# Optimization experiments

Hardware: AMD Instinct MI355X
Metric: run time of the kernel (lower is better)

Reference implementation:

```python
import jax, jax.numpy as jnp
import numpy as np

SHIFT_MIN, SHIFT_MAX = -14.0, 0.0  # weight_bits=5 -> (-(2^4-2), 0)
FRAC_BITS = 16
INT_BITS = 16


def round_to_fixed(x):
    # deepshift utils.round_to_fixed: floor to 2^-16 grid, clamp to [-2^15, 2^15-1]
    delta = 2.0 ** (-FRAC_BITS)
    bound = 2.0 ** (INT_BITS - 1)
    r = jnp.floor(x / delta) * delta
    return jnp.clip(r, -bound, bound - 1)


def setup_inputs() -> dict:
    key = jax.random.key(0)
    k1, k2, k3, k4 = jax.random.split(key, 4)
    N, IN, OUT = 524288, 128, 128
    x = jax.random.normal(k1, (N, IN), dtype=jnp.float32)
    shift = jax.random.uniform(k2, (OUT, IN), dtype=jnp.float32, minval=SHIFT_MIN, maxval=SHIFT_MAX)
    sign = jax.random.uniform(k3, (OUT, IN), dtype=jnp.float32, minval=-1.0, maxval=1.0)
    bound = 1.0 / np.sqrt(IN)
    bias = jax.random.uniform(k4, (OUT,), dtype=jnp.float32, minval=-bound, maxval=bound)
    return {"input": x, "shift": shift, "sign": sign, "bias": bias}


def reference(input, shift, sign, bias):
    # quantize weights: v = 2^round(clamp(shift)) * sign(round(sign))
    shift_r = jnp.round(jnp.clip(shift, SHIFT_MIN, SHIFT_MAX))
    sign_s = jnp.sign(jnp.round(sign))
    v = jnp.exp2(shift_r) * sign_s  # [OUT, IN]
    x_q = round_to_fixed(input)
    b_q = round_to_fixed(bias)
    # F.linear: x @ v.T + b
    return jnp.dot(x_q, v.T) + b_q[None, :]
```

## Files before the change

kernel.cpp:

```cpp
#include <hip/hip_runtime.h>
#include <hip/hip_bf16.h>
#include <stdint.h>

typedef __attribute__((ext_vector_type(4)))  float f32x4;
typedef __attribute__((ext_vector_type(16))) float f32x16;
typedef __attribute__((ext_vector_type(8)))  short bf16x8;

constexpr int IN_DIM  = 128;
constexpr int OUT_DIM = 128;
constexpr int BLOCK   = 256;
constexpr int TILE_ROWS = 32;
constexpr int TILES_PER_BLOCK = 8;
constexpr int ROWS_PER_BLOCK = TILE_ROWS * TILES_PER_BLOCK;
constexpr int NBUF = 3;

__device__ __forceinline__ bf16x8 build_seg(const float* __restrict__ shiftp,
                                            const float* __restrict__ signp,
                                            int row, int j)
{
    const int g = row * IN_DIM + j * 8;
    f32x4 sh0 = *reinterpret_cast<const f32x4*>(shiftp + g);
    f32x4 sh1 = *reinterpret_cast<const f32x4*>(shiftp + g + 4);
    f32x4 sg0 = *reinterpret_cast<const f32x4*>(signp + g);
    f32x4 sg1 = *reinterpret_cast<const f32x4*>(signp + g + 4);
    union { ushort u[8]; bf16x8 v; } tmp;
    #pragma unroll
    for (int e = 0; e < 8; ++e) {
        float sh = (e < 4) ? sh0[e] : sh1[e - 4];
        float sg = (e < 4) ? sg0[e] : sg1[e - 4];
        sh = fminf(fmaxf(sh, -14.0f), 0.0f);
        const int   si = (int)rintf(sh);
        const float rs = rintf(sg);
        ushort bits = 0;
        if (rs != 0.0f)
            bits = (ushort)(((rs < 0.0f) ? 0x8000u : 0u) |
                            (unsigned)((127 + si) << 7));
        tmp.u[e] = bits;
    }
    return tmp.v;
}

__device__ __forceinline__ void stage_tile(const float* __restrict__ gtile,
                                           float* __restrict__ lbuf,
                                           int wave, int lane)
{
    #pragma unroll
    for (int i = 0; i < 4; ++i) {
        const int seg = wave * 4 + i;
        const int p   = seg * 64 + lane;
        const int row = p >> 5;
        const int cl  = p & 31;
        const int cg  = cl ^ (row & 7);
        const float* g = gtile + row * IN_DIM + cg * 4;
        __builtin_amdgcn_global_load_lds(
            (const __attribute__((address_space(1))) unsigned int*)(uintptr_t)g,
            (__attribute__((address_space(3))) unsigned int*)(uintptr_t)(lbuf + seg * 256),
            16, 0, 0);
    }
}

__global__ __launch_bounds__(BLOCK, 3)
void linshift_main(const float* __restrict__ x,
                   const float* __restrict__ shiftp,
                   const float* __restrict__ signp,
                   const float* __restrict__ biasp,
                   float* __restrict__ out)
{
    __shared__ float xbuf[NBUF][TILE_ROWS * IN_DIM];

    const int t    = threadIdx.x;
    const int ct   = t >> 6;
    const int lane = t & 63;
    const int ml   = lane & 31;
    const int hi   = lane >> 5;
    const int o    = ct * 32 + ml;

    bf16x8 vb[8];
    #pragma unroll
    for (int ks = 0; ks < 8; ++ks)
        vb[ks] = build_seg(shiftp, signp, o, ks * 2 + hi);
    const float bv = floorf(biasp[o] * 65536.0f) * (1.0f / 65536.0f);

    const long long brow0 = (long long)blockIdx.x * ROWS_PER_BLOCK;
    const float* xblock = x + brow0 * IN_DIM;

    stage_tile(xblock,                      xbuf[0], ct, lane);
    stage_tile(xblock + TILE_ROWS * IN_DIM, xbuf[1], ct, lane);

    const int swz = ml & 7;
    #pragma unroll
    for (int tl = 0; tl < TILES_PER_BLOCK; ++tl) {
        asm volatile("s_waitcnt vmcnt(4)" ::: "memory");
        __builtin_amdgcn_s_barrier();
        __builtin_amdgcn_sched_barrier(0);

        if (tl + 2 < TILES_PER_BLOCK)
            stage_tile(xblock + (long long)(tl + 2) * TILE_ROWS * IN_DIM,
                       xbuf[(tl + 2) % NBUF], ct, lane);

        const float* buf = xbuf[tl % NBUF];

        bf16x8 a[8];
        #pragma unroll
        for (int ks = 0; ks < 8; ++ks) {
            const int c0 = ks * 4 + hi * 2;
            f32x4 f0 = *reinterpret_cast<const f32x4*>(&buf[ml * IN_DIM + ((c0 ^ swz) << 2)]);
            f32x4 f1 = *reinterpret_cast<const f32x4*>(&buf[ml * IN_DIM + (((c0 + 1) ^ swz) << 2)]);
            union { ushort u[8]; bf16x8 v; } tmp;
            #pragma unroll
            for (int e = 0; e < 4; ++e) {
                __hip_bfloat16 h0 = __float2bfloat16(f0[e]);
                __hip_bfloat16 h1 = __float2bfloat16(f1[e]);
                tmp.u[e]     = *reinterpret_cast<const ushort*>(&h0);
                tmp.u[e + 4] = *reinterpret_cast<const ushort*>(&h1);
            }
            a[ks] = tmp.v;
        }

        f32x16 acc;
        #pragma unroll
        for (int r = 0; r < 16; ++r) acc[r] = bv;
        #pragma unroll
        for (int ks = 0; ks < 8; ++ks)
            acc = __builtin_amdgcn_mfma_f32_32x32x16_bf16(a[ks], vb[ks], acc, 0, 0, 0);

        float* op = out + (brow0 + (long long)tl * TILE_ROWS) * OUT_DIM + o;
        #pragma unroll
        for (int r = 0; r < 16; ++r) {
            const int m = (r & 3) + 8 * (r >> 2) + 4 * hi;
            __builtin_nontemporal_store(acc[r], op + m * OUT_DIM);
        }
        __builtin_amdgcn_sched_barrier(0);
    }
}

extern "C" void kernel_launch(void* const* d_in, const int* in_sizes, int n_in,
                              void* d_out, int out_size, void* d_ws, size_t ws_size,
                              hipStream_t stream) {
    const float* x  = (const float*)d_in[0];
    const float* sh = (const float*)d_in[1];
    const float* sg = (const float*)d_in[2];
    const float* b  = (const float*)d_in[3];
    float* out = (float*)d_out;

    const int N = in_sizes[0] / IN_DIM;
    const int grid = N / ROWS_PER_BLOCK;
    linshift_main<<<grid, BLOCK, 0, stream>>>(x, sh, sg, b, out);
}
```

Baseline: 99.25 us.

## Stage x through registers, convert to bf16 before LDS, double-buffer

```diff
diff --git a/kernel.cpp b/kernel.cpp
--- a/kernel.cpp
+++ b/kernel.cpp
@@ -5,6 +5,7 @@
 typedef __attribute__((ext_vector_type(4)))  float f32x4;
 typedef __attribute__((ext_vector_type(16))) float f32x16;
 typedef __attribute__((ext_vector_type(8)))  short bf16x8;
+typedef __attribute__((ext_vector_type(8)))  ushort u16x8;
 
 constexpr int IN_DIM  = 128;
 constexpr int OUT_DIM = 128;
@@ -12,7 +13,6 @@
 constexpr int TILE_ROWS = 32;
 constexpr int TILES_PER_BLOCK = 8;
 constexpr int ROWS_PER_BLOCK = TILE_ROWS * TILES_PER_BLOCK;
-constexpr int NBUF = 3;
 
 __device__ __forceinline__ bf16x8 build_seg(const float* __restrict__ shiftp,
                                             const float* __restrict__ signp,
@@ -40,33 +40,14 @@
     return tmp.v;
 }
 
-__device__ __forceinline__ void stage_tile(const float* __restrict__ gtile,
-                                           float* __restrict__ lbuf,
-                                           int wave, int lane)
-{
-    #pragma unroll
-    for (int i = 0; i < 4; ++i) {
-        const int seg = wave * 4 + i;
-        const int p   = seg * 64 + lane;
-        const int row = p >> 5;
-        const int cl  = p & 31;
-        const int cg  = cl ^ (row & 7);
-        const float* g = gtile + row * IN_DIM + cg * 4;
-        __builtin_amdgcn_global_load_lds(
-            (const __attribute__((address_space(1))) unsigned int*)(uintptr_t)g,
-            (__attribute__((address_space(3))) unsigned int*)(uintptr_t)(lbuf + seg * 256),
-            16, 0, 0);
-    }
-}
-
-__global__ __launch_bounds__(BLOCK, 3)
+__global__ __launch_bounds__(BLOCK, 4)
 void linshift_main(const float* __restrict__ x,
                    const float* __restrict__ shiftp,
                    const float* __restrict__ signp,
                    const float* __restrict__ biasp,
                    float* __restrict__ out)
 {
-    __shared__ float xbuf[NBUF][TILE_ROWS * IN_DIM];
+    __shared__ ushort buf[2][TILE_ROWS * IN_DIM];
 
     const int t    = threadIdx.x;
     const int ct   = t >> 6;
@@ -84,38 +65,50 @@
     const long long brow0 = (long long)blockIdx.x * ROWS_PER_BLOCK;
     const float* xblock = x + brow0 * IN_DIM;
 
-    stage_tile(xblock,                      xbuf[0], ct, lane);
-    stage_tile(xblock + TILE_ROWS * IN_DIM, xbuf[1], ct, lane);
+    f32x4 gA[4], gB[4];
 
-    const int swz = ml & 7;
-    #pragma unroll
-    for (int tl = 0; tl < TILES_PER_BLOCK; ++tl) {
-        asm volatile("s_waitcnt vmcnt(4)" ::: "memory");
-        __builtin_amdgcn_s_barrier();
-        __builtin_amdgcn_sched_barrier(0);
-
-        if (tl + 2 < TILES_PER_BLOCK)
-            stage_tile(xblock + (long long)(tl + 2) * TILE_ROWS * IN_DIM,
-                       xbuf[(tl + 2) % NBUF], ct, lane);
-
-        const float* buf = xbuf[tl % NBUF];
-
-        bf16x8 a[8];
+    auto load_tile = [&](int tl, f32x4 g[4]) {
+        const float* p = xblock + (long long)tl * TILE_ROWS * IN_DIM;
+        g[0] = *reinterpret_cast<const f32x4*>(p + t * 8);
+        g[1] = *reinterpret_cast<const f32x4*>(p + t * 8 + 4);
+        g[2] = *reinterpret_cast<const f32x4*>(p + (t + 256) * 8);
+        g[3] = *reinterpret_cast<const f32x4*>(p + (t + 256) * 8 + 4);
+    };
+    auto write_tile = [&](int bi, f32x4 g[4]) {
         #pragma unroll
-        for (int ks = 0; ks < 8; ++ks) {
-            const int c0 = ks * 4 + hi * 2;
-            f32x4 f0 = *reinterpret_cast<const f32x4*>(&buf[ml * IN_DIM + ((c0 ^ swz) << 2)]);
-            f32x4 f1 = *reinterpret_cast<const f32x4*>(&buf[ml * IN_DIM + (((c0 + 1) ^ swz) << 2)]);
-            union { ushort u[8]; bf16x8 v; } tmp;
+        for (int i = 0; i < 2; ++i) {
+            const int q   = t + i * 256;
+            const int row = q >> 4;
+            const int c   = q & 15;
+            const int sc  = c ^ (row & 7);
+            union { ushort u[8]; u16x8 v; } tmp;
             #pragma unroll
             for (int e = 0; e < 4; ++e) {
-                __hip_bfloat16 h0 = __float2bfloat16(f0[e]);
-                __hip_bfloat16 h1 = __float2bfloat16(f1[e]);
+                __hip_bfloat16 h0 = __float2bfloat16(g[2 * i][e]);
+                __hip_bfloat16 h1 = __float2bfloat16(g[2 * i + 1][e]);
                 tmp.u[e]     = *reinterpret_cast<const ushort*>(&h0);
                 tmp.u[e + 4] = *reinterpret_cast<const ushort*>(&h1);
             }
-            a[ks] = tmp.v;
+            *reinterpret_cast<u16x8*>(&buf[bi][row * IN_DIM + sc * 8]) = tmp.v;
         }
+    };
+
+    load_tile(0, gA);
+    write_tile(0, gA);
+    load_tile(1, gA);
+    __syncthreads();
+
+    #pragma unroll
+    for (int tl = 0; tl < TILES_PER_BLOCK; ++tl) {
+        if (tl + 2 < TILES_PER_BLOCK) load_tile(tl + 2, gB);
+        __builtin_amdgcn_sched_barrier(0);
+
+        const ushort* bp = buf[tl & 1];
+        bf16x8 a[8];
+        #pragma unroll
+        for (int ks = 0; ks < 8; ++ks)
+            a[ks] = *reinterpret_cast<const bf16x8*>(
+                &bp[ml * IN_DIM + (((ks * 2 + hi) ^ (ml & 7)) * 8)]);
 
         f32x16 acc;
         #pragma unroll
@@ -131,6 +124,12 @@
             __builtin_nontemporal_store(acc[r], op + m * OUT_DIM);
         }
         __builtin_amdgcn_sched_barrier(0);
+
+        if (tl + 1 < TILES_PER_BLOCK) write_tile((tl + 1) & 1, gA);
+        __syncthreads();
+
+        #pragma unroll
+        for (int i = 0; i < 4; ++i) gA[i] = gB[i];
     }
 }
 
```

Measured after the change: 197.7 us. +99.1%, slower.
